# Kernel optimization log

Hardware: AMD Instinct MI355X
Metric: run time of the kernel (lower is better)

Reference implementation:

```python
import jax, jax.numpy as jnp
import numpy as np

N_HEAD = 12
D_MODEL = 768
NEG_FILL = -2.0 ** 32 + 1


def setup_inputs() -> dict:
    key0 = jax.random.key(0)
    ks = jax.random.split(key0, 10)
    B, L, D = 4, 2048, D_MODEL
    std = np.sqrt(2.0 / (D + D)).astype(np.float32)
    return {
        "query": jax.random.normal(ks[0], (B, L, D), jnp.float32),
        "key": jax.random.normal(ks[1], (B, L, D), jnp.float32),
        "Wq": jax.random.normal(ks[2], (D, D), jnp.float32) * std,
        "bq": jax.random.normal(ks[3], (D,), jnp.float32) * 0.02,
        "Wk": jax.random.normal(ks[4], (D, D), jnp.float32) * std,
        "bk": jax.random.normal(ks[5], (D,), jnp.float32) * 0.02,
        "Wv": jax.random.normal(ks[6], (D, D), jnp.float32) * std,
        "bv": jax.random.normal(ks[7], (D,), jnp.float32) * 0.02,
        "gamma": jax.random.normal(ks[8], (D,), jnp.float32),
        "beta": jax.random.normal(ks[9], (D,), jnp.float32) * 0.02,
    }


def _split_heads(x, n_head):
    # torch.cat(torch.chunk(x, n_head, dim=2), dim=0): head-major along batch
    B, L, D = x.shape
    d = D // n_head
    return x.reshape(B, L, n_head, d).transpose(2, 0, 1, 3).reshape(n_head * B, L, d)


def _merge_heads(x, n_head):
    # inverse: torch.cat(torch.chunk(x, n_head, dim=0), dim=2)
    HB, L, d = x.shape
    B = HB // n_head
    return x.reshape(n_head, B, L, d).transpose(1, 2, 0, 3).reshape(B, L, n_head * d)


def reference(query, key, Wq, bq, Wk, bk, Wv, bv, gamma, beta):
    n_head = N_HEAD
    B, Lq, D = query.shape
    Lk = key.shape[1]
    d_k = D // n_head

    Q = jax.nn.relu(jnp.einsum("bld,ed->ble", query, Wq) + bq)
    K = jax.nn.relu(jnp.einsum("bld,ed->ble", key, Wk) + bk)
    V = jax.nn.relu(jnp.einsum("bld,ed->ble", key, Wv) + bv)

    Q_ = _split_heads(Q, n_head)  # [H*B, Lq, d_k]
    K_ = _split_heads(K, n_head)
    V_ = _split_heads(V, n_head)

    scores = jnp.einsum("nqd,nkd->nqk", Q_, K_) / jnp.sqrt(jnp.float32(d_k))

    key_mask = jnp.sign(jnp.abs(jnp.sum(key, axis=-1)))      # [B, Lk]
    key_mask = jnp.tile(key_mask, (n_head, 1))               # [H*B, Lk]
    scores = jnp.where(key_mask[:, None, :] == 0, jnp.float32(NEG_FILL), scores)

    attn = jax.nn.softmax(scores, axis=-1)

    q_mask = jnp.sign(jnp.abs(jnp.sum(query, axis=-1)))      # [B, Lq]
    q_mask = jnp.tile(q_mask, (n_head, 1))                   # [H*B, Lq]
    attn = attn * q_mask[:, :, None]

    out = jnp.einsum("nqk,nkd->nqd", attn, V_)
    out = _merge_heads(out, n_head) + query                  # residual

    # Normalize: torch.var is unbiased (ddof=1)
    mean = jnp.mean(out, axis=-1, keepdims=True)
    var = jnp.var(out, axis=-1, keepdims=True, ddof=1)
    normalized = (out - mean) / jnp.sqrt(var + 1e-5)
    return gamma * normalized + beta
```

## Files before the change

### kernel.cpp

```cpp
#include <hip/hip_runtime.h>


using s16x8 = __attribute__((ext_vector_type(8))) short;
using u16x4 = __attribute__((ext_vector_type(4))) unsigned short;
using f32x4 = __attribute__((ext_vector_type(4))) float;

#define MFMA32(a, b, c) __builtin_amdgcn_mfma_f32_16x16x32_bf16((a), (b), (c), 0, 0, 0)

constexpr float QSCALE = 0.125f * 1.44269504088896340736f;
constexpr float NEG_FILL_S = -1.0e10f;

__device__ __forceinline__ unsigned int cvtpk(float a, float b) {
  unsigned int d;
  asm("v_cvt_pk_bf16_f32 %0, %1, %2" : "=v"(d) : "v"(a), "v"(b));
  return d;
}
__device__ __forceinline__ u16x4 pack4(float x0, float x1, float x2, float x3) {
  union { unsigned int d[2]; u16x4 v; } u;
  u.d[0] = cvtpk(x0, x1);
  u.d[1] = cvtpk(x2, x3);
  return u.v;
}
__device__ __forceinline__ unsigned short f2bf(float f) {
  union { float f; unsigned int u; } v; v.f = f;
  return (unsigned short)((v.u + 0x7FFFu + ((v.u >> 16) & 1u)) >> 16);
}
__device__ __forceinline__ float bf2f(unsigned short s) {
  union { unsigned int u; float f; } v; v.u = ((unsigned int)s) << 16;
  return v.f;
}
__device__ __forceinline__ void gll16(const void* g, void* l) {
  __builtin_amdgcn_global_load_lds(
      (const __attribute__((address_space(1))) unsigned int*)g,
      (__attribute__((address_space(3))) unsigned int*)l, 16, 0, 0);
}

__global__ __launch_bounds__(192) void prepass(
    const float* __restrict__ query, const float* __restrict__ key,
    unsigned short* __restrict__ Qbf, unsigned short* __restrict__ Kbf,
    float* __restrict__ qmask, float* __restrict__ kmaskF) {
  const int row = blockIdx.x, tid = threadIdx.x;
  const int isK = blockIdx.y;
  const float* __restrict__ src = isK ? key : query;
  unsigned short* __restrict__ dst = isK ? Kbf : Qbf;
  const size_t base = (size_t)row * 768 + tid * 4;
  float4 v = *(const float4*)&src[base];
  *(u16x4*)&dst[base] = pack4(v.x, v.y, v.z, v.w);
  float s = (v.x + v.y) + (v.z + v.w);
#pragma unroll
  for (int off = 1; off < 64; off <<= 1) s += __shfl_xor(s, off);
  __shared__ float ws[3];
  if ((tid & 63) == 0) ws[tid >> 6] = s;
  __syncthreads();
  if (tid == 0) {
    float t = ws[0] + ws[1] + ws[2];
    if (isK)
      kmaskF[row] = (t != 0.0f) ? 0.0f : NEG_FILL_S;
    else
      qmask[row] = (t != 0.0f) ? 1.0f : 0.0f;
  }
}

__global__ __launch_bounds__(256) void convw(
    const float* __restrict__ Wq, const float* __restrict__ Wk,
    const float* __restrict__ Wv, unsigned short* __restrict__ Wbf) {
  const float* __restrict__ W = (blockIdx.y == 0) ? Wq : (blockIdx.y == 1) ? Wk : Wv;
  const size_t idx = ((size_t)blockIdx.x * 256 + threadIdx.x) * 4;
  float4 v = *(const float4*)&W[idx];
  *(u16x4*)&Wbf[(size_t)blockIdx.y * 589824 + idx] = pack4(v.x, v.y, v.z, v.w);
}

__global__ __launch_bounds__(256, 3) void proj_qkv(
    const unsigned short* __restrict__ Qbf, const unsigned short* __restrict__ Kbf,
    const unsigned short* __restrict__ Wbf,
    const float* __restrict__ bq, const float* __restrict__ bk,
    const float* __restrict__ bv,
    unsigned short* __restrict__ Qh, unsigned short* __restrict__ Ks,
    unsigned short* __restrict__ Vs) {
  const int lin = blockIdx.x;
  const int swz = (lin & 7) * 288 + (lin >> 3);
  const int z = swz / 768;
  const int rem = swz - z * 768;
  const int m0 = (rem / 12) * 128, n0 = (rem % 12) * 64;
  const unsigned short* __restrict__ A = (z == 0) ? Qbf : Kbf;
  const unsigned short* __restrict__ W = Wbf + (size_t)z * 589824;
  const float* __restrict__ bias = (z == 0) ? bq : (z == 1) ? bk : bv;

  __shared__ unsigned short Al[2][128][64];
  __shared__ unsigned short Bl[2][64][64];

  const int tid = threadIdx.x, lane = tid & 63, wave = tid >> 6;
  const int wm = wave >> 1, wn = wave & 1;
  const int lx = lane & 15, lg = lane >> 4;
  const int sw = lx & 7;

  f32x4 acc[4][2] = {};

  auto stage = [&](int buf, int kt) {
#pragma unroll
    for (int i = 0; i < 4; ++i) {
      const int c = tid + i * 256;
      const int r = c >> 3, cc = c & 7;
      const int scol = kt + ((cc ^ (r & 7)) << 3);
      gll16(&A[(size_t)(m0 + r) * 768 + scol],
            &Al[buf][0][0] + ((size_t)(i * 256 + wave * 64)) * 8);
    }
#pragma unroll
    for (int i = 0; i < 2; ++i) {
      const int c = tid + i * 256;
      const int r = c >> 3, cc = c & 7;
      const int scol = kt + ((cc ^ (r & 7)) << 3);
      gll16(&W[(size_t)(n0 + r) * 768 + scol],
            &Bl[buf][0][0] + ((size_t)(i * 256 + wave * 64)) * 8);
    }
  };

  stage(0, 0);
  asm volatile("s_waitcnt vmcnt(0)" ::: "memory");
  __syncthreads();
  for (int t = 0; t < 12; ++t) {
    if (t < 11) stage((t + 1) & 1, (t + 1) * 64);
    const int buf = t & 1;
#pragma unroll
    for (int kb = 0; kb < 2; ++kb) {
      s16x8 af[4], bfr[2];
#pragma unroll
      for (int i = 0; i < 4; ++i)
        af[i] = *(const s16x8*)&Al[buf][wm * 64 + i * 16 + lx][((kb * 4 + lg) ^ sw) << 3];
#pragma unroll
      for (int j = 0; j < 2; ++j)
        bfr[j] = *(const s16x8*)&Bl[buf][wn * 32 + j * 16 + lx][((kb * 4 + lg) ^ sw) << 3];
#pragma unroll
      for (int i = 0; i < 4; ++i)
#pragma unroll
        for (int j = 0; j < 2; ++j)
          acc[i][j] = MFMA32(af[i], bfr[j], acc[i][j]);
    }
    asm volatile("s_waitcnt vmcnt(0)" ::: "memory");
    __syncthreads();
  }

  const float scale = (z == 0) ? QSCALE : 1.0f;
#pragma unroll
  for (int fm = 0; fm < 4; ++fm) {
#pragma unroll
    for (int fn = 0; fn < 2; ++fn) {
      const int e = n0 + wn * 32 + fn * 16 + lx;
      const int hh = e >> 6, d = e & 63;
      const int mg = m0 + wm * 64 + fm * 16 + (lg << 2);
      const int bb = mg >> 11, l = mg & 2047;
      const int nn = hh * 4 + bb;
      const float bv_ = bias[e];
      if (z == 2) {
        *(u16x4*)&Vs[(((size_t)nn * 512 + (l >> 2)) * 64 + d) * 4] =
            pack4(fmaxf(acc[fm][fn][0] + bv_, 0.0f), fmaxf(acc[fm][fn][1] + bv_, 0.0f),
                  fmaxf(acc[fm][fn][2] + bv_, 0.0f), fmaxf(acc[fm][fn][3] + bv_, 0.0f));
      } else if (z == 1) {
#pragma unroll
        for (int r = 0; r < 4; ++r) {
          float vv = fmaxf(acc[fm][fn][r] + bv_, 0.0f);
          Ks[((((size_t)nn * 128 + (l >> 4)) * 8 + (d >> 3)) * 16 + ((l & 12) + r)) * 8 +
             (d & 7)] = f2bf(vv);
        }
      } else {
#pragma unroll
        for (int r = 0; r < 4; ++r) {
          float vv = fmaxf(acc[fm][fn][r] + bv_, 0.0f) * scale;
          Qh[((size_t)(nn * 2048 + l + r)) * 64 + d] = f2bf(vv);
        }
      }
    }
  }
}

__global__ __launch_bounds__(128, 2) void attn_fwd(
    const unsigned short* __restrict__ Qh, const unsigned short* __restrict__ Ks,
    const unsigned short* __restrict__ Vs, const float* __restrict__ qmask,
    const float* __restrict__ kmaskF, unsigned short* __restrict__ attnw) {
  const int lin = blockIdx.x;
  const int swz = (lin & 7) * 96 + (lin >> 3);
  const int n = swz >> 4;
  const int q0 = (swz & 15) * 128;
  const int h = n >> 2, b = n & 3;
  const int tid = threadIdx.x, lane = tid & 63, wave = tid >> 6;
  const int lx = lane & 15, lg = lane >> 4;
  const int sw = lx & 7;

  __shared__ unsigned short PT[128][64];

  const int qw = q0 + wave * 64;
  s16x8 qf[4][2];
#pragma unroll
  for (int fq = 0; fq < 4; ++fq)
#pragma unroll
    for (int kb = 0; kb < 2; ++kb)
      qf[fq][kb] = *(const s16x8*)&Qh[((size_t)n * 2048 + qw + fq * 16 + lx) * 64 +
                                      kb * 32 + lg * 8];

  const unsigned short* __restrict__ Ksn = Ks + (size_t)n * 131072;
  const unsigned short* __restrict__ Vsn = Vs + (size_t)n * 131072;
  const float* __restrict__ kfp = kmaskF + b * 2048;

  f32x4 o[4][4] = {};
  float lrun[4] = {0.0f, 0.0f, 0.0f, 0.0f};

  for (int t = 0; t < 32; ++t) {
    const int kt = t * 64;

    f32x4 s[4][4] = {};
#pragma unroll
    for (int fkr = 0; fkr < 4; ++fkr) {
      const int rb = t * 4 + fkr;
      s16x8 kf0 = *(const s16x8*)&Ksn[(size_t)(((rb * 8 + lg) * 16) + lx) * 8];
      s16x8 kf1 = *(const s16x8*)&Ksn[(size_t)(((rb * 8 + 4 + lg) * 16) + lx) * 8];
#pragma unroll
      for (int fq = 0; fq < 4; ++fq) {
        s[fkr][fq] = MFMA32(kf0, qf[fq][0], s[fkr][fq]);
        s[fkr][fq] = MFMA32(kf1, qf[fq][1], s[fkr][fq]);
      }
    }

    uint2 vraw[8][2];
#pragma unroll
    for (int kb = 0; kb < 2; ++kb)
#pragma unroll
      for (int fd = 0; fd < 4; ++fd) {
        const int d = fd * 16 + lx;
        const int g0 = (kt >> 2) + kb * 8 + lg * 2;
        const uint2* vp = (const uint2*)&Vsn[(((size_t)g0) * 64 + d) * 4];
        vraw[kb * 4 + fd][0] = vp[0];
        vraw[kb * 4 + fd][1] = vp[64];
      }

    float4 fl[4];
#pragma unroll
    for (int fkr = 0; fkr < 4; ++fkr)
      fl[fkr] = *(const float4*)&kfp[kt + fkr * 16 + lg * 4];

#pragma unroll
    for (int fq = 0; fq < 4; ++fq) {
#pragma unroll
      for (int fkr = 0; fkr < 4; ++fkr) {
        float p0 = __builtin_amdgcn_exp2f(s[fkr][fq][0] + fl[fkr].x);
        float p1 = __builtin_amdgcn_exp2f(s[fkr][fq][1] + fl[fkr].y);
        float p2 = __builtin_amdgcn_exp2f(s[fkr][fq][2] + fl[fkr].z);
        float p3 = __builtin_amdgcn_exp2f(s[fkr][fq][3] + fl[fkr].w);
        lrun[fq] += (p0 + p1) + (p2 + p3);
        const int row = wave * 64 + fq * 16 + lx;
        const int chunk = fkr * 2 + (lg >> 1);
        unsigned short* wp = &PT[row][((chunk ^ sw) << 3) + ((lg & 1) << 2)];
        uint2 pd;
        pd.x = cvtpk(p0, p1);
        pd.y = cvtpk(p2, p3);
        *(uint2*)wp = pd;
      }
    }
    asm volatile("s_waitcnt lgkmcnt(0)" ::: "memory");
    __builtin_amdgcn_sched_barrier(0);

#pragma unroll
    for (int kb = 0; kb < 2; ++kb) {
      s16x8 pf[4];
#pragma unroll
      for (int fq = 0; fq < 4; ++fq)
        pf[fq] = *(const s16x8*)&PT[wave * 64 + fq * 16 + lx][((kb * 4 + lg) ^ sw) << 3];
#pragma unroll
      for (int fd = 0; fd < 4; ++fd) {
        union { uint2 u2[2]; s16x8 v; } vf;
        vf.u2[0] = vraw[kb * 4 + fd][0];
        vf.u2[1] = vraw[kb * 4 + fd][1];
#pragma unroll
        for (int fq = 0; fq < 4; ++fq)
          o[fd][fq] = MFMA32(vf.v, pf[fq], o[fd][fq]);
      }
    }
  }

#pragma unroll
  for (int fq = 0; fq < 4; ++fq) {
    lrun[fq] += __shfl_xor(lrun[fq], 16);
    lrun[fq] += __shfl_xor(lrun[fq], 32);
  }
#pragma unroll
  for (int fd = 0; fd < 4; ++fd)
#pragma unroll
    for (int fq = 0; fq < 4; ++fq) {
      const int qg = qw + fq * 16 + lx;
      const float osc = qmask[b * 2048 + qg] / lrun[fq];
      *(u16x4*)&attnw[((size_t)(b * 2048 + qg)) * 768 + h * 64 + fd * 16 + lg * 4] =
          pack4(o[fd][fq][0] * osc, o[fd][fq][1] * osc, o[fd][fq][2] * osc,
                o[fd][fq][3] * osc);
    }
}

__global__ __launch_bounds__(192) void ln_kernel(
    const unsigned short* __restrict__ attnw, const float* __restrict__ query,
    const float* __restrict__ gamma, const float* __restrict__ beta,
    float* __restrict__ out) {
  const int row = blockIdx.x, tid = threadIdx.x;
  const size_t base = (size_t)row * 768 + tid * 4;
  u16x4 aw = *(const u16x4*)&attnw[base];
  float4 q = *(const float4*)&query[base];
  float x0 = bf2f(aw[0]) + q.x;
  float x1 = bf2f(aw[1]) + q.y;
  float x2 = bf2f(aw[2]) + q.z;
  float x3 = bf2f(aw[3]) + q.w;
  float s = (x0 + x1) + (x2 + x3);
  float s2 = (x0 * x0 + x1 * x1) + (x2 * x2 + x3 * x3);
#pragma unroll
  for (int off = 1; off < 64; off <<= 1) {
    s += __shfl_xor(s, off);
    s2 += __shfl_xor(s2, off);
  }
  __shared__ float ws[3], ws2[3];
  if ((tid & 63) == 0) { ws[tid >> 6] = s; ws2[tid >> 6] = s2; }
  __syncthreads();
  s = ws[0] + ws[1] + ws[2];
  s2 = ws2[0] + ws2[1] + ws2[2];
  const float mean = s * (1.0f / 768.0f);
  const float var = (s2 - 768.0f * mean * mean) * (1.0f / 767.0f);
  const float rstd = rsqrtf(var + 1e-5f);
  const float4 g = *(const float4*)&gamma[tid * 4];
  const float4 bt = *(const float4*)&beta[tid * 4];
  float4 r;
  r.x = g.x * (x0 - mean) * rstd + bt.x;
  r.y = g.y * (x1 - mean) * rstd + bt.y;
  r.z = g.z * (x2 - mean) * rstd + bt.z;
  r.w = g.w * (x3 - mean) * rstd + bt.w;
  *(float4*)&out[base] = r;
}

extern "C" void kernel_launch(void* const* d_in, const int* in_sizes, int n_in,
                              void* d_out, int out_size, void* d_ws, size_t ws_size,
                              hipStream_t stream) {
  const float* query = (const float*)d_in[0];
  const float* key = (const float*)d_in[1];
  const float* Wq = (const float*)d_in[2];
  const float* bq = (const float*)d_in[3];
  const float* Wk = (const float*)d_in[4];
  const float* bk = (const float*)d_in[5];
  const float* Wv = (const float*)d_in[6];
  const float* bv = (const float*)d_in[7];
  const float* gamma = (const float*)d_in[8];
  const float* beta = (const float*)d_in[9];
  float* out = (float*)d_out;

  unsigned short* Qbf = (unsigned short*)d_ws;
  unsigned short* Kbf = Qbf + 6291456;
  unsigned short* Qh = Kbf + 6291456;
  unsigned short* Ks = Qh + 6291456;
  unsigned short* Vs = Ks + 6291456;
  unsigned short* Wbf = Vs + 6291456;
  unsigned short* attnw = Qbf;
  float* qmask = (float*)(Wbf + 1769472);
  float* kmaskF = qmask + 8192;

  convw<<<dim3(576, 3), 256, 0, stream>>>(Wq, Wk, Wv, Wbf);
  prepass<<<dim3(8192, 2), 192, 0, stream>>>(query, key, Qbf, Kbf, qmask, kmaskF);
  proj_qkv<<<2304, 256, 0, stream>>>(Qbf, Kbf, Wbf, bq, bk, bv, Qh, Ks, Vs);
  attn_fwd<<<768, 128, 0, stream>>>(Qh, Ks, Vs, qmask, kmaskF, attnw);
  ln_kernel<<<8192, 192, 0, stream>>>(attnw, query, gamma, beta, out);
}
```

Measured before the change: 244.4 us.

## Split attention key range across waves and merge partials via LDS

Each attention block now handles 64 query rows instead of 128, and its two waves each process half of the key tiles for the same queries. The partial outputs and row sums are combined through shared memory at the end. This doubles the grid to 1536 blocks for better occupancy and load balance across CUs. The cost is that each block reloads K/V for fewer queries, which raises K/V traffic, and it adds an LDS reduction step and extra barriers.

```diff
diff --git a/kernel.cpp b/kernel.cpp
--- a/kernel.cpp
+++ b/kernel.cpp
@@ -178,23 +178,24 @@
     const unsigned short* __restrict__ Vs, const float* __restrict__ qmask,
     const float* __restrict__ kmaskF, unsigned short* __restrict__ attnw) {
   const int lin = blockIdx.x;
-  const int swz = (lin & 7) * 96 + (lin >> 3);
-  const int n = swz >> 4;
-  const int q0 = (swz & 15) * 128;
+  const int swz = (lin & 7) * 192 + (lin >> 3);
+  const int n = swz >> 5;
+  const int q0 = (swz & 31) * 64;
   const int h = n >> 2, b = n & 3;
   const int tid = threadIdx.x, lane = tid & 63, wave = tid >> 6;
   const int lx = lane & 15, lg = lane >> 4;
   const int sw = lx & 7;
 
-  __shared__ unsigned short PT[128][64];
-
-  const int qw = q0 + wave * 64;
+  __shared__ unsigned short PT[140][64];
+  float* XF = (float*)&PT[0][0];
+  __shared__ float lrL[64];
+
   s16x8 qf[4][2];
 #pragma unroll
   for (int fq = 0; fq < 4; ++fq)
 #pragma unroll
     for (int kb = 0; kb < 2; ++kb)
-      qf[fq][kb] = *(const s16x8*)&Qh[((size_t)n * 2048 + qw + fq * 16 + lx) * 64 +
+      qf[fq][kb] = *(const s16x8*)&Qh[((size_t)n * 2048 + q0 + fq * 16 + lx) * 64 +
                                       kb * 32 + lg * 8];
 
   const unsigned short* __restrict__ Ksn = Ks + (size_t)n * 131072;
@@ -204,7 +205,9 @@
   f32x4 o[4][4] = {};
   float lrun[4] = {0.0f, 0.0f, 0.0f, 0.0f};
 
-  for (int t = 0; t < 32; ++t) {
+  const int tbase = wave * 16;
+  for (int tt = 0; tt < 16; ++tt) {
+    const int t = tbase + tt;
     const int kt = t * 64;
 
     f32x4 s[4][4] = {};
@@ -281,16 +284,38 @@
     lrun[fq] += __shfl_xor(lrun[fq], 16);
     lrun[fq] += __shfl_xor(lrun[fq], 32);
   }
-#pragma unroll
-  for (int fd = 0; fd < 4; ++fd)
+
+  __syncthreads();
+  if (wave == 1) {
 #pragma unroll
     for (int fq = 0; fq < 4; ++fq) {
-      const int qg = qw + fq * 16 + lx;
-      const float osc = qmask[b * 2048 + qg] / lrun[fq];
-      *(u16x4*)&attnw[((size_t)(b * 2048 + qg)) * 768 + h * 64 + fd * 16 + lg * 4] =
-          pack4(o[fd][fq][0] * osc, o[fd][fq][1] * osc, o[fd][fq][2] * osc,
-                o[fd][fq][3] * osc);
-    }
+#pragma unroll
+      for (int fd = 0; fd < 4; ++fd)
+        *(float4*)&XF[(fq * 16 + lx) * 68 + fd * 16 + lg * 4] =
+            *(float4*)&o[fd][fq];
+      if (lg == 0) lrL[fq * 16 + lx] = lrun[fq];
+    }
+  }
+  __syncthreads();
+  if (wave == 0) {
+#pragma unroll
+    for (int fq = 0; fq < 4; ++fq) {
+      const float lother = lrL[fq * 16 + lx];
+      const int qg = q0 + fq * 16 + lx;
+      float ltot = lrun[fq] + lother;
+      const float osc = qmask[b * 2048 + qg] / ltot;
+#pragma unroll
+      for (int fd = 0; fd < 4; ++fd) {
+        float4 ov = *(const float4*)&XF[(fq * 16 + lx) * 68 + fd * 16 + lg * 4];
+        float r0 = (o[fd][fq][0] + ov.x) * osc;
+        float r1 = (o[fd][fq][1] + ov.y) * osc;
+        float r2 = (o[fd][fq][2] + ov.z) * osc;
+        float r3 = (o[fd][fq][3] + ov.w) * osc;
+        *(u16x4*)&attnw[((size_t)(b * 2048 + qg)) * 768 + h * 64 + fd * 16 + lg * 4] =
+            pack4(r0, r1, r2, r3);
+      }
+    }
+  }
 }
 
 __global__ __launch_bounds__(192) void ln_kernel(
@@ -358,6 +383,6 @@
   convw<<<dim3(576, 3), 256, 0, stream>>>(Wq, Wk, Wv, Wbf);
   prepass<<<dim3(8192, 2), 192, 0, stream>>>(query, key, Qbf, Kbf, qmask, kmaskF);
   proj_qkv<<<2304, 256, 0, stream>>>(Qbf, Kbf, Wbf, bq, bk, bv, Qh, Ks, Vs);
-  attn_fwd<<<768, 128, 0, stream>>>(Qh, Ks, Vs, qmask, kmaskF, attnw);
+  attn_fwd<<<1536, 128, 0, stream>>>(Qh, Ks, Vs, qmask, kmaskF, attnw);
   ln_kernel<<<8192, 192, 0, stream>>>(attnw, query, gamma, beta, out);
 }
```

New measurement: 257.6 us. +5.4%, slower.
